# Optimization experiments

Measured on AMD Instinct MI355X. Metric: run time of the kernel, lower is better.

Reference implementation:

```python
import jax, jax.numpy as jnp
import numpy as np

N_NODES = 10000
HEADS = 4
NEG_SLOPE = 0.2


def gat_conv(x, src, dst, W, att_src, att_dst, bias, heads, ch):
    # x: [N, F_in]; W: [F_in, heads*ch]; att_*: [heads, ch]; bias: [heads*ch]
    N = x.shape[0]
    h = (x @ W).reshape(N, heads, ch)                       # [N, H, C]
    a_s = jnp.einsum('nhc,hc->nh', h, att_src)              # [N, H]
    a_d = jnp.einsum('nhc,hc->nh', h, att_dst)              # [N, H]
    e = jax.nn.leaky_relu(a_s[src] + a_d[dst], NEG_SLOPE)   # [E, H]
    # segment softmax over incoming edges of each dst node
    m = jax.ops.segment_max(e, dst, num_segments=N)         # [N, H]
    e = jnp.exp(e - m[dst])
    denom = jax.ops.segment_sum(e, dst, num_segments=N)     # [N, H]
    alpha = e / (denom[dst] + 1e-16)                        # [E, H]
    msg = h[src] * alpha[:, :, None]                        # [E, H, C]
    out = jax.ops.segment_sum(msg, dst, num_segments=N)     # [N, H, C]
    return out.reshape(N, heads * ch) + bias                # concat heads


def setup_inputs() -> dict:
    key = jax.random.key(0)
    ks = jax.random.split(key, 12)
    in_c, hid, out_c, H = 256, 64, 64, HEADS
    n_edges = 320000
    x = jax.random.normal(ks[0], (N_NODES, in_c), dtype=jnp.float32)
    edge_index = jax.random.randint(ks[1], (2, n_edges), 0, N_NODES, dtype=jnp.int64)

    def glorot(k, shape):
        fan = shape[0] + shape[-1]
        s = jnp.sqrt(6.0 / fan)
        return jax.random.uniform(k, shape, jnp.float32, -s, s)

    return {
        'x': x, 'edge_index': edge_index,
        'W1': glorot(ks[2], (in_c, H * hid)),
        'a1s': glorot(ks[3], (H, hid)), 'a1d': glorot(ks[4], (H, hid)),
        'b1': jnp.zeros((H * hid,), jnp.float32),
        'W2': glorot(ks[5], (H * hid, H * hid)),
        'a2s': glorot(ks[6], (H, hid)), 'a2d': glorot(ks[7], (H, hid)),
        'b2': jnp.zeros((H * hid,), jnp.float32),
        'W3': glorot(ks[8], (H * hid, H * out_c)),
        'a3s': glorot(ks[9], (H, out_c)), 'a3d': glorot(ks[10], (H, out_c)),
        'b3': jnp.zeros((H * out_c,), jnp.float32),
    }


def reference(x, edge_index, W1, a1s, a1d, b1, W2, a2s, a2d, b2, W3, a3s, a3d, b3):
    N = x.shape[0]
    # PyG GATConv default: add self loops
    loops = jnp.arange(N, dtype=edge_index.dtype)
    src = jnp.concatenate([edge_index[0], loops])
    dst = jnp.concatenate([edge_index[1], loops])
    hid, out_c = 64, 64
    h1 = jax.nn.elu(gat_conv(x, src, dst, W1, a1s, a1d, b1, HEADS, hid))
    h2 = jax.nn.elu(gat_conv(h1, src, dst, W2, a2s, a2d, b2, HEADS, hid))
    oup = jax.nn.elu(gat_conv(h2, src, dst, W3, a3s, a3d, b3, HEADS, out_c))
    return oup
```

## Files before the change

kernel.cpp:

```cpp
#include <hip/hip_runtime.h>
#include <hip/hip_bf16.h>

typedef __hip_bfloat16 bf16;
typedef __bf16 bf16x8v __attribute__((ext_vector_type(8)));
typedef float f32x4 __attribute__((ext_vector_type(4)));
typedef unsigned short u16x8 __attribute__((ext_vector_type(8)));

#define CAP 128

__device__ __forceinline__ float bits2f(unsigned short u) {
  union { unsigned int i; float f; } c;
  c.i = ((unsigned int)u) << 16;
  return c.f;
}


__global__ void wt_zero_kernel(const float* __restrict__ W0, const float* __restrict__ W1,
                               const float* __restrict__ W2, bf16* __restrict__ Wt,
                               int* __restrict__ cnt, int N) {
  __shared__ float tile[16][17];
  int b = blockIdx.x;
  if (b < 768) {
    int L = b >> 8, rem = b & 255;
    const float* W = (L == 0) ? W0 : (L == 1) ? W1 : W2;
    bf16* T = Wt + (size_t)L * 65536;
    int n0 = (rem & 15) * 16, k0 = (rem >> 4) * 16;
    int tx = threadIdx.x & 15, ty = threadIdx.x >> 4;
    tile[ty][tx] = W[(k0 + ty) * 256 + n0 + tx];
    __syncthreads();
    T[(n0 + ty) * 256 + k0 + tx] = __float2bfloat16(tile[tx][ty]);
  } else {
    int idx = (b - 768) * 256 + threadIdx.x;
    if (idx < N) cnt[idx] = 0;
  }
}


template <bool FP32IN>
__device__ __forceinline__ void gemm_body(const void* __restrict__ Xv,
                                          const bf16* __restrict__ Wt,
                                          const float* __restrict__ att_s,
                                          const float* __restrict__ att_d,
                                          bf16* __restrict__ H, float* __restrict__ a_s,
                                          float* __restrict__ a_d, int M, int m0, int hd,
                                          bf16* As, bf16* Bs) {
  const int LDK = 136;
  int tid = threadIdx.x;
  int wave = tid >> 6, lane = tid & 63;
  int quad = lane >> 4, l16 = lane & 15;
  int n0 = hd * 64;
  int srow = tid >> 2;
  int koff = (tid & 3) * 32;

  const float* Xf = (const float*)Xv;
  const bf16*  Xb = (const bf16*)Xv;

  f32x4 acc[4] = {{0.f, 0.f, 0.f, 0.f}, {0.f, 0.f, 0.f, 0.f},
                  {0.f, 0.f, 0.f, 0.f}, {0.f, 0.f, 0.f, 0.f}};

  for (int ks = 0; ks < 256; ks += 128) {
    int gm = m0 + srow;
#pragma unroll
    for (int c = 0; c < 4; c++) {
      int ko = koff + c * 8;
      uint4 v;
      if (FP32IN) {
        float4 u0 = make_float4(0.f, 0.f, 0.f, 0.f), u1 = u0;
        if (gm < M) {
          u0 = *(const float4*)&Xf[gm * 256 + ks + ko];
          u1 = *(const float4*)&Xf[gm * 256 + ks + ko + 4];
        }
        union { bf16 h[8]; uint4 u; } pk;
        pk.h[0] = __float2bfloat16(u0.x); pk.h[1] = __float2bfloat16(u0.y);
        pk.h[2] = __float2bfloat16(u0.z); pk.h[3] = __float2bfloat16(u0.w);
        pk.h[4] = __float2bfloat16(u1.x); pk.h[5] = __float2bfloat16(u1.y);
        pk.h[6] = __float2bfloat16(u1.z); pk.h[7] = __float2bfloat16(u1.w);
        v = pk.u;
      } else {
        v = (gm < M) ? *(const uint4*)&Xb[gm * 256 + ks + ko]
                     : make_uint4(0u, 0u, 0u, 0u);
      }
      *(uint4*)&As[srow * LDK + ko] = v;
    }
#pragma unroll
    for (int c = 0; c < 4; c++) {
      int ko = koff + c * 8;
      *(uint4*)&Bs[srow * LDK + ko] = *(const uint4*)&Wt[(n0 + srow) * 256 + ks + ko];
    }
    __syncthreads();

#pragma unroll
    for (int kk = 0; kk < 4; kk++) {
      bf16x8v af = *(const bf16x8v*)&As[(wave * 16 + l16) * LDK + kk * 32 + quad * 8];
#pragma unroll
      for (int t = 0; t < 4; t++) {
        bf16x8v bfr = *(const bf16x8v*)&Bs[(t * 16 + l16) * LDK + kk * 32 + quad * 8];
        acc[t] = __builtin_amdgcn_mfma_f32_16x16x32_bf16(af, bfr, acc[t], 0, 0, 0);
      }
    }
    __syncthreads();
  }

  float ps[4] = {0.f, 0.f, 0.f, 0.f}, pd[4] = {0.f, 0.f, 0.f, 0.f};
#pragma unroll
  for (int t = 0; t < 4; t++) {
    float sa = att_s[hd * 64 + t * 16 + l16];
    float da = att_d[hd * 64 + t * 16 + l16];
#pragma unroll
    for (int j = 0; j < 4; j++) {
      int gm = m0 + wave * 16 + quad * 4 + j;
      float v = acc[t][j];
      if (gm < M) H[gm * 256 + n0 + t * 16 + l16] = __float2bfloat16(v);
      ps[j] += v * sa;
      pd[j] += v * da;
    }
  }
#pragma unroll
  for (int j = 0; j < 4; j++) {
#pragma unroll
    for (int s = 1; s < 16; s <<= 1) {
      ps[j] += __shfl_xor(ps[j], s, 64);
      pd[j] += __shfl_xor(pd[j], s, 64);
    }
    int gm = m0 + wave * 16 + quad * 4 + j;
    if (l16 == 0 && gm < M) {
      a_s[gm * 4 + hd] = ps[j];
      a_d[gm * 4 + hd] = pd[j];
    }
  }
}

__global__ void __launch_bounds__(256, 4)
gemm_mfma_kernel(const bf16* __restrict__ X, const bf16* __restrict__ Wt,
                 const float* __restrict__ att_s, const float* __restrict__ att_d,
                 bf16* __restrict__ H, float* __restrict__ a_s, float* __restrict__ a_d,
                 int M) {
  __shared__ bf16 As[64 * 136];
  __shared__ bf16 Bs[64 * 136];
  gemm_body<false>(X, Wt, att_s, att_d, H, a_s, a_d, M, blockIdx.x * 64, blockIdx.y,
                   As, Bs);
}

__global__ void __launch_bounds__(256, 4)
gemm1_fill_kernel(const float* __restrict__ X, const bf16* __restrict__ Wt,
                  const float* __restrict__ att_s, const float* __restrict__ att_d,
                  bf16* __restrict__ H, float* __restrict__ a_s, float* __restrict__ a_d,
                  int M, const int* __restrict__ ei, int E, int N,
                  int* __restrict__ cnt, int* __restrict__ csr, int ngb) {
  __shared__ bf16 As[64 * 136];
  __shared__ bf16 Bs[64 * 136];
  int b = blockIdx.x;
  if (b < ngb) {
    gemm_body<true>(X, Wt, att_s, att_d, H, a_s, a_d, M, (b >> 2) * 64, b & 3, As, Bs);
  } else {
    int t = (b - ngb) * 256 + threadIdx.x;
    if (t >= E + N) return;
    int src, dst;
    if (t < E) { src = ei[t]; dst = ei[E + t]; }
    else       { src = t - E; dst = t - E; }
    int pos = atomicAdd(&cnt[dst], 1);
    if (pos < CAP) csr[dst * CAP + pos] = src;
  }
}


template <bool FINAL>
__global__ void __launch_bounds__(256, 8)
agg_wave_kernel(const bf16* __restrict__ H, const float* __restrict__ a_s,
                const float* __restrict__ a_d, const int* __restrict__ cnt,
                const int* __restrict__ csr, const float* __restrict__ bias,
                bf16* __restrict__ OutB, float* __restrict__ OutF, int N) {
  __shared__ int   wIdx[4][128];
  __shared__ float wP[4][128 * 4];
  int tid = threadIdx.x;
  int wave = tid >> 6, lane = tid & 63;
  int n = blockIdx.x * 4 + wave;

  int deg = 0, degp = 0;
  if (n < N) {
    deg = min(cnt[n], CAP);
    degp = (deg + 7) & ~7;
    float4 ad4 = *(const float4*)&a_d[n * 4];
#pragma unroll
    for (int base = 0; base < 2; base++) {
      int jj = base * 64 + lane;
      if (jj < deg) {
        int src = csr[n * CAP + jj];
        wIdx[wave][jj] = src;
        float4 as4 = *(const float4*)&a_s[src * 4];
        float4 e;
        e.x = as4.x + ad4.x; e.x = (e.x > 0.f) ? e.x : 0.2f * e.x;
        e.y = as4.y + ad4.y; e.y = (e.y > 0.f) ? e.y : 0.2f * e.y;
        e.z = as4.z + ad4.z; e.z = (e.z > 0.f) ? e.z : 0.2f * e.z;
        e.w = as4.w + ad4.w; e.w = (e.w > 0.f) ? e.w : 0.2f * e.w;
        float4 pv;
        pv.x = __expf(e.x); pv.y = __expf(e.y);
        pv.z = __expf(e.z); pv.w = __expf(e.w);
        *(float4*)&wP[wave][jj * 4] = pv;
      }
    }
    int pad = degp - deg;
    if (lane < pad) {
      int jd = deg + lane;
      wIdx[wave][jd] = 0;
      *(float4*)&wP[wave][jd * 4] = make_float4(0.f, 0.f, 0.f, 0.f);
    }
  }
  __syncthreads();
  if (n >= N) return;

  int sel = lane >> 5;
  int l32 = lane & 31;
  int c8 = l32 * 8;
  int head = l32 >> 3;
  const unsigned short* Hs = (const unsigned short*)H;

  float acc[8] = {0.f, 0.f, 0.f, 0.f, 0.f, 0.f, 0.f, 0.f};
  float s = 0.f;
  int npairp = degp >> 1;

  for (int it = 0; it < npairp; it += 4) {
    int   jv[4]; int sv[4]; float pv[4]; u16x8 hv[4];
#pragma unroll
    for (int u = 0; u < 4; u++) jv[u] = 2 * (it + u) + sel;
#pragma unroll
    for (int u = 0; u < 4; u++) sv[u] = wIdx[wave][jv[u]];
#pragma unroll
    for (int u = 0; u < 4; u++) pv[u] = wP[wave][jv[u] * 4 + head];
#pragma unroll
    for (int u = 0; u < 4; u++) hv[u] = *(const u16x8*)(Hs + sv[u] * 256 + c8);
#pragma unroll
    for (int u = 0; u < 4; u++) {
      s += pv[u];
#pragma unroll
      for (int k = 0; k < 8; k++) acc[k] += pv[u] * bits2f(hv[u][k]);
    }
  }

  s += __shfl_xor(s, 32, 64);
#pragma unroll
  for (int k = 0; k < 8; k++) acc[k] += __shfl_xor(acc[k], 32, 64);

  if (sel == 0) {
    float inv = 1.f / (s + 1e-16f);
    float4 b0 = *(const float4*)&bias[c8];
    float4 b1 = *(const float4*)&bias[c8 + 4];
    float v[8];
    v[0] = acc[0] * inv + b0.x; v[1] = acc[1] * inv + b0.y;
    v[2] = acc[2] * inv + b0.z; v[3] = acc[3] * inv + b0.w;
    v[4] = acc[4] * inv + b1.x; v[5] = acc[5] * inv + b1.y;
    v[6] = acc[6] * inv + b1.z; v[7] = acc[7] * inv + b1.w;
#pragma unroll
    for (int k = 0; k < 8; k++) v[k] = (v[k] > 0.f) ? v[k] : expm1f(v[k]);
    if (FINAL) {
      *(float4*)&OutF[n * 256 + c8]     = make_float4(v[0], v[1], v[2], v[3]);
      *(float4*)&OutF[n * 256 + c8 + 4] = make_float4(v[4], v[5], v[6], v[7]);
    } else {
      union { bf16 h[8]; u16x8 u; } pk;
#pragma unroll
      for (int k = 0; k < 8; k++) pk.h[k] = __float2bfloat16(v[k]);
      *(u16x8*)((unsigned short*)OutB + n * 256 + c8) = pk.u;
    }
  }
}


extern "C" void kernel_launch(void* const* d_in, const int* in_sizes, int n_in,
                              void* d_out, int out_size, void* d_ws, size_t ws_size,
                              hipStream_t stream) {
  const int N = in_sizes[0] / 256;
  const int E = in_sizes[1] / 2;

  const float* x  = (const float*)d_in[0];
  const int*   ei = (const int*)d_in[1];
  const float* Wl[3]  = {(const float*)d_in[2], (const float*)d_in[6], (const float*)d_in[10]};
  const float* asl[3] = {(const float*)d_in[3], (const float*)d_in[7], (const float*)d_in[11]};
  const float* adl[3] = {(const float*)d_in[4], (const float*)d_in[8], (const float*)d_in[12]};
  const float* bl[3]  = {(const float*)d_in[5], (const float*)d_in[9], (const float*)d_in[13]};
  float* out = (float*)d_out;

  char* p = (char*)d_ws;
  auto carve = [&](size_t bytes) {
    char* r = p;
    p += (bytes + 255) & ~size_t(255);
    return r;
  };
  int*   cnt     = (int*)carve(sizeof(int) * N);
  int*   csr     = (int*)carve(sizeof(int) * N * CAP);
  float* a_s     = (float*)carve(sizeof(float) * N * 4);
  float* a_d     = (float*)carve(sizeof(float) * N * 4);
  bf16*  Wt      = (bf16*)carve(sizeof(bf16) * 3 * 65536);
  bf16*  h_buf   = (bf16*)carve(sizeof(bf16) * N * 256);
  bf16*  x_buf   = (bf16*)carve(sizeof(bf16) * N * 256);
  (void)ws_size; (void)n_in; (void)out_size;

  const int zb = (N + 255) / 256;
  const int eb = (E + N + 255) / 256;
  const int ngb = ((N + 63) / 64) * 4;
  const int ab = (N + 3) / 4;
  dim3 ggrid((N + 63) / 64, 4);

  wt_zero_kernel<<<768 + zb, 256, 0, stream>>>(Wl[0], Wl[1], Wl[2], Wt, cnt, N);
  gemm1_fill_kernel<<<ngb + eb, 256, 0, stream>>>(x, Wt, asl[0], adl[0], h_buf,
                                                  a_s, a_d, N, ei, E, N, cnt, csr, ngb);
  agg_wave_kernel<false><<<ab, 256, 0, stream>>>(h_buf, a_s, a_d, cnt, csr, bl[0],
                                                 x_buf, nullptr, N);
  gemm_mfma_kernel<<<ggrid, 256, 0, stream>>>(x_buf, Wt + 65536, asl[1], adl[1],
                                              h_buf, a_s, a_d, N);
  agg_wave_kernel<false><<<ab, 256, 0, stream>>>(h_buf, a_s, a_d, cnt, csr, bl[1],
                                                 x_buf, nullptr, N);
  gemm_mfma_kernel<<<ggrid, 256, 0, stream>>>(x_buf, Wt + 131072, asl[2], adl[2],
                                              h_buf, a_s, a_d, N);
  agg_wave_kernel<true><<<ab, 256, 0, stream>>>(h_buf, a_s, a_d, cnt, csr, bl[2],
                                                nullptr, out, N);
}
```

Baseline: 189.0 us.

## Fuse all GAT stages into one persistent cooperative kernel with grid syncs

```diff
diff --git a/kernel.cpp b/kernel.cpp
--- a/kernel.cpp
+++ b/kernel.cpp
@@ -1,5 +1,8 @@
 #include <hip/hip_runtime.h>
+#include <hip/hip_cooperative_groups.h>
 #include <hip/hip_bf16.h>
+
+namespace cg = cooperative_groups;
 
 typedef __hip_bfloat16 bf16;
 typedef __bf16 bf16x8v __attribute__((ext_vector_type(8)));
@@ -12,27 +15,6 @@
   union { unsigned int i; float f; } c;
   c.i = ((unsigned int)u) << 16;
   return c.f;
-}
-
-
-__global__ void wt_zero_kernel(const float* __restrict__ W0, const float* __restrict__ W1,
-                               const float* __restrict__ W2, bf16* __restrict__ Wt,
-                               int* __restrict__ cnt, int N) {
-  __shared__ float tile[16][17];
-  int b = blockIdx.x;
-  if (b < 768) {
-    int L = b >> 8, rem = b & 255;
-    const float* W = (L == 0) ? W0 : (L == 1) ? W1 : W2;
-    bf16* T = Wt + (size_t)L * 65536;
-    int n0 = (rem & 15) * 16, k0 = (rem >> 4) * 16;
-    int tx = threadIdx.x & 15, ty = threadIdx.x >> 4;
-    tile[ty][tx] = W[(k0 + ty) * 256 + n0 + tx];
-    __syncthreads();
-    T[(n0 + ty) * 256 + k0 + tx] = __float2bfloat16(tile[tx][ty]);
-  } else {
-    int idx = (b - 768) * 256 + threadIdx.x;
-    if (idx < N) cnt[idx] = 0;
-  }
 }
 
 
@@ -127,6 +109,210 @@
       a_s[gm * 4 + hd] = ps[j];
       a_d[gm * 4 + hd] = pd[j];
     }
+  }
+}
+
+
+__device__ __forceinline__ void agg_stage(const bf16* __restrict__ H,
+                                          const float* __restrict__ a_s,
+                                          const float* __restrict__ a_d,
+                                          const int* __restrict__ cnt,
+                                          const int* __restrict__ csr,
+                                          const float* __restrict__ bias,
+                                          bf16* __restrict__ OutB,
+                                          float* __restrict__ OutF, int N,
+                                          bool final_, char* smem, int blk, int nblk) {
+  int tid = threadIdx.x;
+  int wave = tid >> 6, lane = tid & 63;
+  int* wIdx = (int*)smem + wave * 128;
+  float* wP = (float*)(smem + 2048) + wave * 512;
+  int ngr = (N + 3) >> 2;
+  for (int ng = blk; ng < ngr; ng += nblk) {
+    int n = ng * 4 + wave;
+    int deg = 0, degp = 0;
+    if (n < N) {
+      deg = min(cnt[n], CAP);
+      degp = (deg + 7) & ~7;
+      float4 ad4 = *(const float4*)&a_d[n * 4];
+#pragma unroll
+      for (int base = 0; base < 2; base++) {
+        int jj = base * 64 + lane;
+        if (jj < deg) {
+          int src = csr[n * CAP + jj];
+          wIdx[jj] = src;
+          float4 as4 = *(const float4*)&a_s[src * 4];
+          float4 e;
+          e.x = as4.x + ad4.x; e.x = (e.x > 0.f) ? e.x : 0.2f * e.x;
+          e.y = as4.y + ad4.y; e.y = (e.y > 0.f) ? e.y : 0.2f * e.y;
+          e.z = as4.z + ad4.z; e.z = (e.z > 0.f) ? e.z : 0.2f * e.z;
+          e.w = as4.w + ad4.w; e.w = (e.w > 0.f) ? e.w : 0.2f * e.w;
+          float4 pv;
+          pv.x = __expf(e.x); pv.y = __expf(e.y);
+          pv.z = __expf(e.z); pv.w = __expf(e.w);
+          *(float4*)&wP[jj * 4] = pv;
+        }
+      }
+      int pad = degp - deg;
+      if (lane < pad) {
+        wIdx[deg + lane] = 0;
+        *(float4*)&wP[(deg + lane) * 4] = make_float4(0.f, 0.f, 0.f, 0.f);
+      }
+    }
+    __syncthreads();
+    if (n < N) {
+      int sel = lane >> 5;
+      int l32 = lane & 31;
+      int c8 = l32 * 8;
+      int head = l32 >> 3;
+      const unsigned short* Hs = (const unsigned short*)H;
+
+      float acc[8] = {0.f, 0.f, 0.f, 0.f, 0.f, 0.f, 0.f, 0.f};
+      float s = 0.f;
+      int npairp = degp >> 1;
+
+      for (int it = 0; it < npairp; it += 4) {
+        int jv[4]; int sv[4]; float pv[4]; u16x8 hv[4];
+#pragma unroll
+        for (int u = 0; u < 4; u++) jv[u] = 2 * (it + u) + sel;
+#pragma unroll
+        for (int u = 0; u < 4; u++) sv[u] = wIdx[jv[u]];
+#pragma unroll
+        for (int u = 0; u < 4; u++) pv[u] = wP[jv[u] * 4 + head];
+#pragma unroll
+        for (int u = 0; u < 4; u++) hv[u] = *(const u16x8*)(Hs + sv[u] * 256 + c8);
+#pragma unroll
+        for (int u = 0; u < 4; u++) {
+          s += pv[u];
+#pragma unroll
+          for (int k = 0; k < 8; k++) acc[k] += pv[u] * bits2f(hv[u][k]);
+        }
+      }
+
+      s += __shfl_xor(s, 32, 64);
+#pragma unroll
+      for (int k = 0; k < 8; k++) acc[k] += __shfl_xor(acc[k], 32, 64);
+
+      if (sel == 0) {
+        float inv = 1.f / (s + 1e-16f);
+        float4 b0 = *(const float4*)&bias[c8];
+        float4 b1 = *(const float4*)&bias[c8 + 4];
+        float v[8];
+        v[0] = acc[0] * inv + b0.x; v[1] = acc[1] * inv + b0.y;
+        v[2] = acc[2] * inv + b0.z; v[3] = acc[3] * inv + b0.w;
+        v[4] = acc[4] * inv + b1.x; v[5] = acc[5] * inv + b1.y;
+        v[6] = acc[6] * inv + b1.z; v[7] = acc[7] * inv + b1.w;
+#pragma unroll
+        for (int k = 0; k < 8; k++) v[k] = (v[k] > 0.f) ? v[k] : expm1f(v[k]);
+        if (final_) {
+          *(float4*)&OutF[n * 256 + c8]     = make_float4(v[0], v[1], v[2], v[3]);
+          *(float4*)&OutF[n * 256 + c8 + 4] = make_float4(v[4], v[5], v[6], v[7]);
+        } else {
+          union { bf16 h[8]; u16x8 u; } pk;
+#pragma unroll
+          for (int k = 0; k < 8; k++) pk.h[k] = __float2bfloat16(v[k]);
+          *(u16x8*)((unsigned short*)OutB + n * 256 + c8) = pk.u;
+        }
+      }
+    }
+  }
+}
+
+
+__global__ void __launch_bounds__(256, 4)
+uber_kernel(const float* __restrict__ x, const int* __restrict__ ei,
+            const float* __restrict__ W0, const float* __restrict__ as0,
+            const float* __restrict__ ad0, const float* __restrict__ bias0,
+            const float* __restrict__ W1, const float* __restrict__ as1,
+            const float* __restrict__ ad1, const float* __restrict__ bias1,
+            const float* __restrict__ W2, const float* __restrict__ as2,
+            const float* __restrict__ ad2, const float* __restrict__ bias2,
+            int* __restrict__ cnt, int* __restrict__ csr,
+            float* __restrict__ a_s, float* __restrict__ a_d,
+            bf16* __restrict__ Wt, bf16* __restrict__ h_buf,
+            bf16* __restrict__ x_buf, float* __restrict__ outp, int N, int E) {
+  cg::grid_group grid = cg::this_grid();
+  __shared__ char smem[34816];
+  bf16* As = (bf16*)smem;
+  bf16* Bs = (bf16*)smem + 64 * 136;
+  int nblk = (int)gridDim.x;
+  int blk = (int)blockIdx.x;
+  int tid = threadIdx.x;
+
+  {
+    float(*tile)[17] = (float(*)[17])smem;
+    int zb = (N + 255) >> 8;
+    for (int b = blk; b < 768 + zb; b += nblk) {
+      if (b < 768) {
+        int L = b >> 8, rem = b & 255;
+        const float* W = (L == 0) ? W0 : (L == 1) ? W1 : W2;
+        bf16* T = Wt + (size_t)L * 65536;
+        int n0 = (rem & 15) * 16, k0 = (rem >> 4) * 16;
+        int tx = tid & 15, ty = tid >> 4;
+        tile[ty][tx] = W[(k0 + ty) * 256 + n0 + tx];
+        __syncthreads();
+        T[(n0 + ty) * 256 + k0 + tx] = __float2bfloat16(tile[tx][ty]);
+      } else {
+        int idx = (b - 768) * 256 + tid;
+        if (idx < N) cnt[idx] = 0;
+      }
+      __syncthreads();
+    }
+  }
+  grid.sync();
+
+  int ngb = ((N + 63) >> 6) * 4;
+  for (int j = blk; j < ngb; j += nblk)
+    gemm_body<true>(x, Wt, as0, ad0, h_buf, a_s, a_d, N, (j >> 2) * 64, j & 3, As, Bs);
+  int eb = (E + N + 255) >> 8;
+  for (int j = blk; j < eb; j += nblk) {
+    int t = j * 256 + tid;
+    if (t < E + N) {
+      int s_, d_;
+      if (t < E) { s_ = ei[t]; d_ = ei[E + t]; }
+      else       { s_ = t - E; d_ = t - E; }
+      int pos = atomicAdd(&cnt[d_], 1);
+      if (pos < CAP) csr[d_ * CAP + pos] = s_;
+    }
+  }
+  grid.sync();
+
+  agg_stage(h_buf, a_s, a_d, cnt, csr, bias0, x_buf, nullptr, N, false, smem, blk, nblk);
+  grid.sync();
+
+  for (int j = blk; j < ngb; j += nblk)
+    gemm_body<false>(x_buf, Wt + 65536, as1, ad1, h_buf, a_s, a_d, N, (j >> 2) * 64,
+                     j & 3, As, Bs);
+  grid.sync();
+
+  agg_stage(h_buf, a_s, a_d, cnt, csr, bias1, x_buf, nullptr, N, false, smem, blk, nblk);
+  grid.sync();
+
+  for (int j = blk; j < ngb; j += nblk)
+    gemm_body<false>(x_buf, Wt + 131072, as2, ad2, h_buf, a_s, a_d, N, (j >> 2) * 64,
+                     j & 3, As, Bs);
+  grid.sync();
+
+  agg_stage(h_buf, a_s, a_d, cnt, csr, bias2, nullptr, outp, N, true, smem, blk, nblk);
+}
+
+
+__global__ void wt_zero_kernel(const float* __restrict__ W0, const float* __restrict__ W1,
+                               const float* __restrict__ W2, bf16* __restrict__ Wt,
+                               int* __restrict__ cnt, int N) {
+  __shared__ float tile[16][17];
+  int b = blockIdx.x;
+  if (b < 768) {
+    int L = b >> 8, rem = b & 255;
+    const float* W = (L == 0) ? W0 : (L == 1) ? W1 : W2;
+    bf16* T = Wt + (size_t)L * 65536;
+    int n0 = (rem & 15) * 16, k0 = (rem >> 4) * 16;
+    int tx = threadIdx.x & 15, ty = threadIdx.x >> 4;
+    tile[ty][tx] = W[(k0 + ty) * 256 + n0 + tx];
+    __syncthreads();
+    T[(n0 + ty) * 256 + k0 + tx] = __float2bfloat16(tile[tx][ty]);
+  } else {
+    int idx = (b - 768) * 256 + threadIdx.x;
+    if (idx < N) cnt[idx] = 0;
   }
 }
 
@@ -163,105 +349,15 @@
   }
 }
 
-
 template <bool FINAL>
 __global__ void __launch_bounds__(256, 8)
 agg_wave_kernel(const bf16* __restrict__ H, const float* __restrict__ a_s,
                 const float* __restrict__ a_d, const int* __restrict__ cnt,
                 const int* __restrict__ csr, const float* __restrict__ bias,
                 bf16* __restrict__ OutB, float* __restrict__ OutF, int N) {
-  __shared__ int   wIdx[4][128];
-  __shared__ float wP[4][128 * 4];
-  int tid = threadIdx.x;
-  int wave = tid >> 6, lane = tid & 63;
-  int n = blockIdx.x * 4 + wave;
-
-  int deg = 0, degp = 0;
-  if (n < N) {
-    deg = min(cnt[n], CAP);
-    degp = (deg + 7) & ~7;
-    float4 ad4 = *(const float4*)&a_d[n * 4];
-#pragma unroll
-    for (int base = 0; base < 2; base++) {
-      int jj = base * 64 + lane;
-      if (jj < deg) {
-        int src = csr[n * CAP + jj];
-        wIdx[wave][jj] = src;
-        float4 as4 = *(const float4*)&a_s[src * 4];
-        float4 e;
-        e.x = as4.x + ad4.x; e.x = (e.x > 0.f) ? e.x : 0.2f * e.x;
-        e.y = as4.y + ad4.y; e.y = (e.y > 0.f) ? e.y : 0.2f * e.y;
-        e.z = as4.z + ad4.z; e.z = (e.z > 0.f) ? e.z : 0.2f * e.z;
-        e.w = as4.w + ad4.w; e.w = (e.w > 0.f) ? e.w : 0.2f * e.w;
-        float4 pv;
-        pv.x = __expf(e.x); pv.y = __expf(e.y);
-        pv.z = __expf(e.z); pv.w = __expf(e.w);
-        *(float4*)&wP[wave][jj * 4] = pv;
-      }
-    }
-    int pad = degp - deg;
-    if (lane < pad) {
-      int jd = deg + lane;
-      wIdx[wave][jd] = 0;
-      *(float4*)&wP[wave][jd * 4] = make_float4(0.f, 0.f, 0.f, 0.f);
-    }
-  }
-  __syncthreads();
-  if (n >= N) return;
-
-  int sel = lane >> 5;
-  int l32 = lane & 31;
-  int c8 = l32 * 8;
-  int head = l32 >> 3;
-  const unsigned short* Hs = (const unsigned short*)H;
-
-  float acc[8] = {0.f, 0.f, 0.f, 0.f, 0.f, 0.f, 0.f, 0.f};
-  float s = 0.f;
-  int npairp = degp >> 1;
-
-  for (int it = 0; it < npairp; it += 4) {
-    int   jv[4]; int sv[4]; float pv[4]; u16x8 hv[4];
-#pragma unroll
-    for (int u = 0; u < 4; u++) jv[u] = 2 * (it + u) + sel;
-#pragma unroll
-    for (int u = 0; u < 4; u++) sv[u] = wIdx[wave][jv[u]];
-#pragma unroll
-    for (int u = 0; u < 4; u++) pv[u] = wP[wave][jv[u] * 4 + head];
-#pragma unroll
-    for (int u = 0; u < 4; u++) hv[u] = *(const u16x8*)(Hs + sv[u] * 256 + c8);
-#pragma unroll
-    for (int u = 0; u < 4; u++) {
-      s += pv[u];
-#pragma unroll
-      for (int k = 0; k < 8; k++) acc[k] += pv[u] * bits2f(hv[u][k]);
-    }
-  }
-
-  s += __shfl_xor(s, 32, 64);
-#pragma unroll
-  for (int k = 0; k < 8; k++) acc[k] += __shfl_xor(acc[k], 32, 64);
-
-  if (sel == 0) {
-    float inv = 1.f / (s + 1e-16f);
-    float4 b0 = *(const float4*)&bias[c8];
-    float4 b1 = *(const float4*)&bias[c8 + 4];
-    float v[8];
-    v[0] = acc[0] * inv + b0.x; v[1] = acc[1] * inv + b0.y;
-    v[2] = acc[2] * inv + b0.z; v[3] = acc[3] * inv + b0.w;
-    v[4] = acc[4] * inv + b1.x; v[5] = acc[5] * inv + b1.y;
-    v[6] = acc[6] * inv + b1.z; v[7] = acc[7] * inv + b1.w;
-#pragma unroll
-    for (int k = 0; k < 8; k++) v[k] = (v[k] > 0.f) ? v[k] : expm1f(v[k]);
-    if (FINAL) {
-      *(float4*)&OutF[n * 256 + c8]     = make_float4(v[0], v[1], v[2], v[3]);
-      *(float4*)&OutF[n * 256 + c8 + 4] = make_float4(v[4], v[5], v[6], v[7]);
-    } else {
-      union { bf16 h[8]; u16x8 u; } pk;
-#pragma unroll
-      for (int k = 0; k < 8; k++) pk.h[k] = __float2bfloat16(v[k]);
-      *(u16x8*)((unsigned short*)OutB + n * 256 + c8) = pk.u;
-    }
-  }
+  __shared__ char smem[10240];
+  agg_stage(H, a_s, a_d, cnt, csr, bias, OutB, OutF, N, FINAL, smem, blockIdx.x,
+            gridDim.x);
 }
 
 
@@ -273,10 +369,18 @@
 
   const float* x  = (const float*)d_in[0];
   const int*   ei = (const int*)d_in[1];
-  const float* Wl[3]  = {(const float*)d_in[2], (const float*)d_in[6], (const float*)d_in[10]};
-  const float* asl[3] = {(const float*)d_in[3], (const float*)d_in[7], (const float*)d_in[11]};
-  const float* adl[3] = {(const float*)d_in[4], (const float*)d_in[8], (const float*)d_in[12]};
-  const float* bl[3]  = {(const float*)d_in[5], (const float*)d_in[9], (const float*)d_in[13]};
+  const float* W0 = (const float*)d_in[2];
+  const float* as0 = (const float*)d_in[3];
+  const float* ad0 = (const float*)d_in[4];
+  const float* bz0 = (const float*)d_in[5];
+  const float* W1 = (const float*)d_in[6];
+  const float* as1 = (const float*)d_in[7];
+  const float* ad1 = (const float*)d_in[8];
+  const float* bz1 = (const float*)d_in[9];
+  const float* W2 = (const float*)d_in[10];
+  const float* as2 = (const float*)d_in[11];
+  const float* ad2 = (const float*)d_in[12];
+  const float* bz2 = (const float*)d_in[13];
   float* out = (float*)d_out;
 
   char* p = (char*)d_ws;
@@ -285,14 +389,36 @@
     p += (bytes + 255) & ~size_t(255);
     return r;
   };
-  int*   cnt     = (int*)carve(sizeof(int) * N);
-  int*   csr     = (int*)carve(sizeof(int) * N * CAP);
-  float* a_s     = (float*)carve(sizeof(float) * N * 4);
-  float* a_d     = (float*)carve(sizeof(float) * N * 4);
-  bf16*  Wt      = (bf16*)carve(sizeof(bf16) * 3 * 65536);
-  bf16*  h_buf   = (bf16*)carve(sizeof(bf16) * N * 256);
-  bf16*  x_buf   = (bf16*)carve(sizeof(bf16) * N * 256);
+  int*   cnt   = (int*)carve(sizeof(int) * N);
+  int*   csr   = (int*)carve(sizeof(int) * N * CAP);
+  float* a_s   = (float*)carve(sizeof(float) * N * 4);
+  float* a_d   = (float*)carve(sizeof(float) * N * 4);
+  bf16*  Wt    = (bf16*)carve(sizeof(bf16) * 3 * 65536);
+  bf16*  h_buf = (bf16*)carve(sizeof(bf16) * N * 256);
+  bf16*  x_buf = (bf16*)carve(sizeof(bf16) * N * 256);
   (void)ws_size; (void)n_in; (void)out_size;
+
+  int nb = 0;
+  if (hipOccupancyMaxActiveBlocksPerMultiprocessor(&nb, uber_kernel, 256, 0) !=
+          hipSuccess || nb < 1)
+    nb = 4;
+  if (nb > 4) nb = 4;
+  int devCU = 0, dev = 0;
+  hipGetDevice(&dev);
+  if (hipDeviceGetAttribute(&devCU, hipDeviceAttributeMultiprocessorCount, dev) !=
+          hipSuccess || devCU <= 0)
+    devCU = 256;
+  int gridX = devCU * nb;
+
+  int Ni = N, Ei = E;
+  void* args[] = {(void*)&x,   (void*)&ei,  (void*)&W0,  (void*)&as0, (void*)&ad0,
+                  (void*)&bz0, (void*)&W1,  (void*)&as1, (void*)&ad1, (void*)&bz1,
+                  (void*)&W2,  (void*)&as2, (void*)&ad2, (void*)&bz2, (void*)&cnt,
+                  (void*)&csr, (void*)&a_s, (void*)&a_d, (void*)&Wt,  (void*)&h_buf,
+                  (void*)&x_buf, (void*)&out, (void*)&Ni, (void*)&Ei};
+  hipError_t cerr = hipLaunchCooperativeKernel((const void*)uber_kernel, dim3(gridX),
+                                               dim3(256), args, 0, stream);
+  if (cerr == hipSuccess) return;
 
   const int zb = (N + 255) / 256;
   const int eb = (E + N + 255) / 256;
@@ -300,17 +426,17 @@
   const int ab = (N + 3) / 4;
   dim3 ggrid((N + 63) / 64, 4);
 
-  wt_zero_kernel<<<768 + zb, 256, 0, stream>>>(Wl[0], Wl[1], Wl[2], Wt, cnt, N);
-  gemm1_fill_kernel<<<ngb + eb, 256, 0, stream>>>(x, Wt, asl[0], adl[0], h_buf,
-                                                  a_s, a_d, N, ei, E, N, cnt, csr, ngb);
-  agg_wave_kernel<false><<<ab, 256, 0, stream>>>(h_buf, a_s, a_d, cnt, csr, bl[0],
-                                                 x_buf, nullptr, N);
-  gemm_mfma_kernel<<<ggrid, 256, 0, stream>>>(x_buf, Wt + 65536, asl[1], adl[1],
-                                              h_buf, a_s, a_d, N);
-  agg_wave_kernel<false><<<ab, 256, 0, stream>>>(h_buf, a_s, a_d, cnt, csr, bl[1],
-                                                 x_buf, nullptr, N);
-  gemm_mfma_kernel<<<ggrid, 256, 0, stream>>>(x_buf, Wt + 131072, asl[2], adl[2],
-                                              h_buf, a_s, a_d, N);
-  agg_wave_kernel<true><<<ab, 256, 0, stream>>>(h_buf, a_s, a_d, cnt, csr, bl[2],
-                                                nullptr, out, N);
-}
+  wt_zero_kernel<<<768 + zb, 256, 0, stream>>>(W0, W1, W2, Wt, cnt, N);
+  gemm1_fill_kernel<<<ngb + eb, 256, 0, stream>>>(x, Wt, as0, ad0, h_buf, a_s, a_d, N,
+                                                  ei, E, N, cnt, csr, ngb);
+  agg_wave_kernel<false><<<ab, 256, 0, stream>>>(h_buf, a_s, a_d, cnt, csr, bz0, x_buf,
+                                                 nullptr, N);
+  gemm_mfma_kernel<<<ggrid, 256, 0, stream>>>(x_buf, Wt + 65536, as1, ad1, h_buf, a_s,
+                                              a_d, N);
+  agg_wave_kernel<false><<<ab, 256, 0, stream>>>(h_buf, a_s, a_d, cnt, csr, bz1, x_buf,
+                                                 nullptr, N);
+  gemm_mfma_kernel<<<ggrid, 256, 0, stream>>>(x_buf, Wt + 131072, as2, ad2, h_buf, a_s,
+                                              a_d, N);
+  agg_wave_kernel<true><<<ab, 256, 0, stream>>>(h_buf, a_s, a_d, cnt, csr, bz2, nullptr,
+                                                out, N);
+}
```

Measured after the change: 601.7 us. +218.3%, slower.

## Fuse aggregation of layer L with GEMM of layer L+1 in one kernel

Applied to the files above, without the earlier changes.

```diff
diff --git a/kernel.cpp b/kernel.cpp
--- a/kernel.cpp
+++ b/kernel.cpp
@@ -128,17 +128,6 @@
       a_d[gm * 4 + hd] = pd[j];
     }
   }
-}
-
-__global__ void __launch_bounds__(256, 4)
-gemm_mfma_kernel(const bf16* __restrict__ X, const bf16* __restrict__ Wt,
-                 const float* __restrict__ att_s, const float* __restrict__ att_d,
-                 bf16* __restrict__ H, float* __restrict__ a_s, float* __restrict__ a_d,
-                 int M) {
-  __shared__ bf16 As[64 * 136];
-  __shared__ bf16 Bs[64 * 136];
-  gemm_body<false>(X, Wt, att_s, att_d, H, a_s, a_d, M, blockIdx.x * 64, blockIdx.y,
-                   As, Bs);
 }
 
 __global__ void __launch_bounds__(256, 4)
@@ -164,17 +153,175 @@
 }
 
 
-template <bool FINAL>
+__global__ void __launch_bounds__(256, 2)
+fused_ag_kernel(const bf16* __restrict__ Hin, const float* __restrict__ as_in,
+                const float* __restrict__ ad_in, const int* __restrict__ cnt,
+                const int* __restrict__ csr, const float* __restrict__ bias,
+                const bf16* __restrict__ Wtn, const float* __restrict__ att_s,
+                const float* __restrict__ att_d, bf16* __restrict__ Hout,
+                float* __restrict__ as_out, float* __restrict__ ad_out, int N) {
+  const int LDKF = 264;
+  const int LDK = 136;
+  __shared__ bf16 As[64 * 264];
+  __shared__ bf16 Bs[64 * 136];
+  int tid = threadIdx.x;
+  int wave = tid >> 6, lane = tid & 63;
+  int m0 = blockIdx.x * 64;
+
+  int*   wIdx = (int*)((char*)Bs + (size_t)wave * 512);
+  float* wP   = (float*)((char*)Bs + 2048 + (size_t)wave * 2048);
+  int sel = lane >> 5, l32 = lane & 31;
+  int c8 = l32 * 8, head = l32 >> 3;
+  const unsigned short* Hs = (const unsigned short*)Hin;
+
+  for (int r = 0; r < 16; r++) {
+    int n = m0 + r * 4 + wave;
+    int deg = 0, degp = 0;
+    if (n < N) {
+      deg = min(cnt[n], CAP);
+      degp = (deg + 7) & ~7;
+      float4 ad4 = *(const float4*)&ad_in[n * 4];
+#pragma unroll
+      for (int base = 0; base < 2; base++) {
+        int jj = base * 64 + lane;
+        if (jj < deg) {
+          int src = csr[n * CAP + jj];
+          wIdx[jj] = src;
+          float4 as4 = *(const float4*)&as_in[src * 4];
+          float4 e;
+          e.x = as4.x + ad4.x; e.x = (e.x > 0.f) ? e.x : 0.2f * e.x;
+          e.y = as4.y + ad4.y; e.y = (e.y > 0.f) ? e.y : 0.2f * e.y;
+          e.z = as4.z + ad4.z; e.z = (e.z > 0.f) ? e.z : 0.2f * e.z;
+          e.w = as4.w + ad4.w; e.w = (e.w > 0.f) ? e.w : 0.2f * e.w;
+          float4 pv;
+          pv.x = __expf(e.x); pv.y = __expf(e.y);
+          pv.z = __expf(e.z); pv.w = __expf(e.w);
+          *(float4*)&wP[jj * 4] = pv;
+        }
+      }
+      int pad = degp - deg;
+      if (lane < pad) {
+        wIdx[deg + lane] = 0;
+        *(float4*)&wP[(deg + lane) * 4] = make_float4(0.f, 0.f, 0.f, 0.f);
+      }
+    }
+    __syncthreads();
+    if (n < N) {
+      float acc[8] = {0.f, 0.f, 0.f, 0.f, 0.f, 0.f, 0.f, 0.f};
+      float s = 0.f;
+      int npairp = degp >> 1;
+      for (int it = 0; it < npairp; it += 4) {
+        int jv[4]; int sv[4]; float pv[4]; u16x8 hv[4];
+#pragma unroll
+        for (int u = 0; u < 4; u++) jv[u] = 2 * (it + u) + sel;
+#pragma unroll
+        for (int u = 0; u < 4; u++) sv[u] = wIdx[jv[u]];
+#pragma unroll
+        for (int u = 0; u < 4; u++) pv[u] = wP[jv[u] * 4 + head];
+#pragma unroll
+        for (int u = 0; u < 4; u++) hv[u] = *(const u16x8*)(Hs + sv[u] * 256 + c8);
+#pragma unroll
+        for (int u = 0; u < 4; u++) {
+          s += pv[u];
+#pragma unroll
+          for (int k = 0; k < 8; k++) acc[k] += pv[u] * bits2f(hv[u][k]);
+        }
+      }
+      s += __shfl_xor(s, 32, 64);
+#pragma unroll
+      for (int k = 0; k < 8; k++) acc[k] += __shfl_xor(acc[k], 32, 64);
+      if (sel == 0) {
+        float inv = 1.f / (s + 1e-16f);
+        float4 b0 = *(const float4*)&bias[c8];
+        float4 b1 = *(const float4*)&bias[c8 + 4];
+        float v[8];
+        v[0] = acc[0] * inv + b0.x; v[1] = acc[1] * inv + b0.y;
+        v[2] = acc[2] * inv + b0.z; v[3] = acc[3] * inv + b0.w;
+        v[4] = acc[4] * inv + b1.x; v[5] = acc[5] * inv + b1.y;
+        v[6] = acc[6] * inv + b1.z; v[7] = acc[7] * inv + b1.w;
+#pragma unroll
+        for (int k = 0; k < 8; k++) v[k] = (v[k] > 0.f) ? v[k] : expm1f(v[k]);
+        union { bf16 h[8]; u16x8 u; } pk;
+#pragma unroll
+        for (int k = 0; k < 8; k++) pk.h[k] = __float2bfloat16(v[k]);
+        *(u16x8*)&As[(r * 4 + wave) * LDKF + c8] = pk.u;
+      }
+    } else if (sel == 0) {
+      u16x8 z = {0, 0, 0, 0, 0, 0, 0, 0};
+      *(u16x8*)&As[(r * 4 + wave) * LDKF + c8] = z;
+    }
+    __syncthreads();
+  }
+
+  int quad = lane >> 4, l16 = lane & 15;
+  int srow = tid >> 2;
+  int koff = (tid & 3) * 32;
+
+  for (int hd = 0; hd < 4; hd++) {
+    int n0 = hd * 64;
+    f32x4 acc[4] = {{0.f, 0.f, 0.f, 0.f}, {0.f, 0.f, 0.f, 0.f},
+                    {0.f, 0.f, 0.f, 0.f}, {0.f, 0.f, 0.f, 0.f}};
+    for (int ks = 0; ks < 256; ks += 128) {
+#pragma unroll
+      for (int c = 0; c < 4; c++) {
+        int ko = koff + c * 8;
+        *(uint4*)&Bs[srow * LDK + ko] = *(const uint4*)&Wtn[(n0 + srow) * 256 + ks + ko];
+      }
+      __syncthreads();
+#pragma unroll
+      for (int kk = 0; kk < 4; kk++) {
+        bf16x8v af = *(const bf16x8v*)&As[(wave * 16 + l16) * LDKF + ks + kk * 32 + quad * 8];
+#pragma unroll
+        for (int t = 0; t < 4; t++) {
+          bf16x8v bfr = *(const bf16x8v*)&Bs[(t * 16 + l16) * LDK + kk * 32 + quad * 8];
+          acc[t] = __builtin_amdgcn_mfma_f32_16x16x32_bf16(af, bfr, acc[t], 0, 0, 0);
+        }
+      }
+      __syncthreads();
+    }
+    float ps[4] = {0.f, 0.f, 0.f, 0.f}, pd[4] = {0.f, 0.f, 0.f, 0.f};
+#pragma unroll
+    for (int t = 0; t < 4; t++) {
+      float sa = att_s[hd * 64 + t * 16 + l16];
+      float da = att_d[hd * 64 + t * 16 + l16];
+#pragma unroll
+      for (int j = 0; j < 4; j++) {
+        int gm = m0 + wave * 16 + quad * 4 + j;
+        float v = acc[t][j];
+        if (gm < N) Hout[gm * 256 + n0 + t * 16 + l16] = __float2bfloat16(v);
+        ps[j] += v * sa;
+        pd[j] += v * da;
+      }
+    }
+#pragma unroll
+    for (int j = 0; j < 4; j++) {
+#pragma unroll
+      for (int s = 1; s < 16; s <<= 1) {
+        ps[j] += __shfl_xor(ps[j], s, 64);
+        pd[j] += __shfl_xor(pd[j], s, 64);
+      }
+      int gm = m0 + wave * 16 + quad * 4 + j;
+      if (l16 == 0 && gm < N) {
+        as_out[gm * 4 + hd] = ps[j];
+        ad_out[gm * 4 + hd] = pd[j];
+      }
+    }
+  }
+}
+
+
 __global__ void __launch_bounds__(256, 8)
-agg_wave_kernel(const bf16* __restrict__ H, const float* __restrict__ a_s,
-                const float* __restrict__ a_d, const int* __restrict__ cnt,
-                const int* __restrict__ csr, const float* __restrict__ bias,
-                bf16* __restrict__ OutB, float* __restrict__ OutF, int N) {
-  __shared__ int   wIdx[4][128];
-  __shared__ float wP[4][128 * 4];
+agg_final_kernel(const bf16* __restrict__ H, const float* __restrict__ a_s,
+                 const float* __restrict__ a_d, const int* __restrict__ cnt,
+                 const int* __restrict__ csr, const float* __restrict__ bias,
+                 float* __restrict__ OutF, int N) {
+  __shared__ int   wIdxS[4][128];
+  __shared__ float wPS[4][512];
   int tid = threadIdx.x;
   int wave = tid >> 6, lane = tid & 63;
   int n = blockIdx.x * 4 + wave;
+  int* wIdx = wIdxS[wave];
+  float* wP = wPS[wave];
 
   int deg = 0, degp = 0;
   if (n < N) {
@@ -186,7 +333,7 @@
       int jj = base * 64 + lane;
       if (jj < deg) {
         int src = csr[n * CAP + jj];
-        wIdx[wave][jj] = src;
+        wIdx[jj] = src;
         float4 as4 = *(const float4*)&a_s[src * 4];
         float4 e;
         e.x = as4.x + ad4.x; e.x = (e.x > 0.f) ? e.x : 0.2f * e.x;
@@ -196,14 +343,13 @@
         float4 pv;
         pv.x = __expf(e.x); pv.y = __expf(e.y);
         pv.z = __expf(e.z); pv.w = __expf(e.w);
-        *(float4*)&wP[wave][jj * 4] = pv;
+        *(float4*)&wP[jj * 4] = pv;
       }
     }
     int pad = degp - deg;
     if (lane < pad) {
-      int jd = deg + lane;
-      wIdx[wave][jd] = 0;
-      *(float4*)&wP[wave][jd * 4] = make_float4(0.f, 0.f, 0.f, 0.f);
+      wIdx[deg + lane] = 0;
+      *(float4*)&wP[(deg + lane) * 4] = make_float4(0.f, 0.f, 0.f, 0.f);
     }
   }
   __syncthreads();
@@ -220,13 +366,13 @@
   int npairp = degp >> 1;
 
   for (int it = 0; it < npairp; it += 4) {
-    int   jv[4]; int sv[4]; float pv[4]; u16x8 hv[4];
+    int jv[4]; int sv[4]; float pv[4]; u16x8 hv[4];
 #pragma unroll
     for (int u = 0; u < 4; u++) jv[u] = 2 * (it + u) + sel;
 #pragma unroll
-    for (int u = 0; u < 4; u++) sv[u] = wIdx[wave][jv[u]];
-#pragma unroll
-    for (int u = 0; u < 4; u++) pv[u] = wP[wave][jv[u] * 4 + head];
+    for (int u = 0; u < 4; u++) sv[u] = wIdx[jv[u]];
+#pragma unroll
+    for (int u = 0; u < 4; u++) pv[u] = wP[jv[u] * 4 + head];
 #pragma unroll
     for (int u = 0; u < 4; u++) hv[u] = *(const u16x8*)(Hs + sv[u] * 256 + c8);
 #pragma unroll
@@ -252,15 +398,8 @@
     v[6] = acc[6] * inv + b1.z; v[7] = acc[7] * inv + b1.w;
 #pragma unroll
     for (int k = 0; k < 8; k++) v[k] = (v[k] > 0.f) ? v[k] : expm1f(v[k]);
-    if (FINAL) {
-      *(float4*)&OutF[n * 256 + c8]     = make_float4(v[0], v[1], v[2], v[3]);
-      *(float4*)&OutF[n * 256 + c8 + 4] = make_float4(v[4], v[5], v[6], v[7]);
-    } else {
-      union { bf16 h[8]; u16x8 u; } pk;
-#pragma unroll
-      for (int k = 0; k < 8; k++) pk.h[k] = __float2bfloat16(v[k]);
-      *(u16x8*)((unsigned short*)OutB + n * 256 + c8) = pk.u;
-    }
+    *(float4*)&OutF[n * 256 + c8]     = make_float4(v[0], v[1], v[2], v[3]);
+    *(float4*)&OutF[n * 256 + c8 + 4] = make_float4(v[4], v[5], v[6], v[7]);
   }
 }
 
@@ -285,32 +424,31 @@
     p += (bytes + 255) & ~size_t(255);
     return r;
   };
-  int*   cnt     = (int*)carve(sizeof(int) * N);
-  int*   csr     = (int*)carve(sizeof(int) * N * CAP);
-  float* a_s     = (float*)carve(sizeof(float) * N * 4);
-  float* a_d     = (float*)carve(sizeof(float) * N * 4);
-  bf16*  Wt      = (bf16*)carve(sizeof(bf16) * 3 * 65536);
-  bf16*  h_buf   = (bf16*)carve(sizeof(bf16) * N * 256);
-  bf16*  x_buf   = (bf16*)carve(sizeof(bf16) * N * 256);
+  int*   cnt   = (int*)carve(sizeof(int) * N);
+  int*   csr   = (int*)carve(sizeof(int) * N * CAP);
+  float* a_s   = (float*)carve(sizeof(float) * N * 4);
+  float* a_d   = (float*)carve(sizeof(float) * N * 4);
+  float* a_s2  = (float*)carve(sizeof(float) * N * 4);
+  float* a_d2  = (float*)carve(sizeof(float) * N * 4);
+  bf16*  Wt    = (bf16*)carve(sizeof(bf16) * 3 * 65536);
+  bf16*  h_buf = (bf16*)carve(sizeof(bf16) * N * 256);
+  bf16*  h2buf = (bf16*)carve(sizeof(bf16) * N * 256);
   (void)ws_size; (void)n_in; (void)out_size;
 
   const int zb = (N + 255) / 256;
   const int eb = (E + N + 255) / 256;
   const int ngb = ((N + 63) / 64) * 4;
+  const int fb = (N + 63) / 64;
   const int ab = (N + 3) / 4;
-  dim3 ggrid((N + 63) / 64, 4);
 
   wt_zero_kernel<<<768 + zb, 256, 0, stream>>>(Wl[0], Wl[1], Wl[2], Wt, cnt, N);
   gemm1_fill_kernel<<<ngb + eb, 256, 0, stream>>>(x, Wt, asl[0], adl[0], h_buf,
                                                   a_s, a_d, N, ei, E, N, cnt, csr, ngb);
-  agg_wave_kernel<false><<<ab, 256, 0, stream>>>(h_buf, a_s, a_d, cnt, csr, bl[0],
-                                                 x_buf, nullptr, N);
-  gemm_mfma_kernel<<<ggrid, 256, 0, stream>>>(x_buf, Wt + 65536, asl[1], adl[1],
-                                              h_buf, a_s, a_d, N);
-  agg_wave_kernel<false><<<ab, 256, 0, stream>>>(h_buf, a_s, a_d, cnt, csr, bl[1],
-                                                 x_buf, nullptr, N);
-  gemm_mfma_kernel<<<ggrid, 256, 0, stream>>>(x_buf, Wt + 131072, asl[2], adl[2],
-                                              h_buf, a_s, a_d, N);
-  agg_wave_kernel<true><<<ab, 256, 0, stream>>>(h_buf, a_s, a_d, cnt, csr, bl[2],
-                                                nullptr, out, N);
-}
+  fused_ag_kernel<<<fb, 256, 0, stream>>>(h_buf, a_s, a_d, cnt, csr, bl[0],
+                                          Wt + 65536, asl[1], adl[1],
+                                          h2buf, a_s2, a_d2, N);
+  fused_ag_kernel<<<fb, 256, 0, stream>>>(h2buf, a_s2, a_d2, cnt, csr, bl[1],
+                                          Wt + 131072, asl[2], adl[2],
+                                          h_buf, a_s, a_d, N);
+  agg_final_kernel<<<ab, 256, 0, stream>>>(h_buf, a_s, a_d, cnt, csr, bl[2], out, N);
+}
```

Result: slower. 288.7 us (+52.7%).

## Fold weight transpose into first GEMM launch and drop agg block barrier

Applied to the files above, without the earlier changes.

```diff
diff --git a/kernel.cpp b/kernel.cpp
--- a/kernel.cpp
+++ b/kernel.cpp
@@ -15,30 +15,9 @@
 }
 
 
-__global__ void wt_zero_kernel(const float* __restrict__ W0, const float* __restrict__ W1,
-                               const float* __restrict__ W2, bf16* __restrict__ Wt,
-                               int* __restrict__ cnt, int N) {
-  __shared__ float tile[16][17];
-  int b = blockIdx.x;
-  if (b < 768) {
-    int L = b >> 8, rem = b & 255;
-    const float* W = (L == 0) ? W0 : (L == 1) ? W1 : W2;
-    bf16* T = Wt + (size_t)L * 65536;
-    int n0 = (rem & 15) * 16, k0 = (rem >> 4) * 16;
-    int tx = threadIdx.x & 15, ty = threadIdx.x >> 4;
-    tile[ty][tx] = W[(k0 + ty) * 256 + n0 + tx];
-    __syncthreads();
-    T[(n0 + ty) * 256 + k0 + tx] = __float2bfloat16(tile[tx][ty]);
-  } else {
-    int idx = (b - 768) * 256 + threadIdx.x;
-    if (idx < N) cnt[idx] = 0;
-  }
-}
-
-
-template <bool FP32IN>
+template <bool FP32IN, bool WF32>
 __device__ __forceinline__ void gemm_body(const void* __restrict__ Xv,
-                                          const bf16* __restrict__ Wt,
+                                          const void* __restrict__ Wv,
                                           const float* __restrict__ att_s,
                                           const float* __restrict__ att_d,
                                           bf16* __restrict__ H, float* __restrict__ a_s,
@@ -54,6 +33,8 @@
 
   const float* Xf = (const float*)Xv;
   const bf16*  Xb = (const bf16*)Xv;
+  const float* Wf = (const float*)Wv;
+  const bf16*  Wb = (const bf16*)Wv;
 
   f32x4 acc[4] = {{0.f, 0.f, 0.f, 0.f}, {0.f, 0.f, 0.f, 0.f},
                   {0.f, 0.f, 0.f, 0.f}, {0.f, 0.f, 0.f, 0.f}};
@@ -82,10 +63,19 @@
       }
       *(uint4*)&As[srow * LDK + ko] = v;
     }
-#pragma unroll
-    for (int c = 0; c < 4; c++) {
-      int ko = koff + c * 8;
-      *(uint4*)&Bs[srow * LDK + ko] = *(const uint4*)&Wt[(n0 + srow) * 256 + ks + ko];
+    if (WF32) {
+      int tn = tid & 63, kq = tid >> 6;
+#pragma unroll
+      for (int i = 0; i < 32; i++) {
+        int kk2 = kq * 32 + i;
+        Bs[tn * LDK + kk2] = __float2bfloat16(Wf[(size_t)(ks + kk2) * 256 + n0 + tn]);
+      }
+    } else {
+#pragma unroll
+      for (int c = 0; c < 4; c++) {
+        int ko = koff + c * 8;
+        *(uint4*)&Bs[srow * LDK + ko] = *(const uint4*)&Wb[(n0 + srow) * 256 + ks + ko];
+      }
     }
     __syncthreads();
 
@@ -137,22 +127,26 @@
                  int M) {
   __shared__ bf16 As[64 * 136];
   __shared__ bf16 Bs[64 * 136];
-  gemm_body<false>(X, Wt, att_s, att_d, H, a_s, a_d, M, blockIdx.x * 64, blockIdx.y,
-                   As, Bs);
+  gemm_body<false, false>(X, Wt, att_s, att_d, H, a_s, a_d, M, blockIdx.x * 64,
+                          blockIdx.y, As, Bs);
 }
 
 __global__ void __launch_bounds__(256, 4)
-gemm1_fill_kernel(const float* __restrict__ X, const bf16* __restrict__ Wt,
+gemm1_fill_kernel(const float* __restrict__ X, const float* __restrict__ W0,
                   const float* __restrict__ att_s, const float* __restrict__ att_d,
                   bf16* __restrict__ H, float* __restrict__ a_s, float* __restrict__ a_d,
                   int M, const int* __restrict__ ei, int E, int N,
-                  int* __restrict__ cnt, int* __restrict__ csr, int ngb) {
+                  int* __restrict__ cnt, int* __restrict__ csr, int ngb, int eb,
+                  const float* __restrict__ W1, const float* __restrict__ W2,
+                  bf16* __restrict__ Wt) {
   __shared__ bf16 As[64 * 136];
   __shared__ bf16 Bs[64 * 136];
+  __shared__ float tile[16][17];
   int b = blockIdx.x;
   if (b < ngb) {
-    gemm_body<true>(X, Wt, att_s, att_d, H, a_s, a_d, M, (b >> 2) * 64, b & 3, As, Bs);
-  } else {
+    gemm_body<true, true>(X, W0, att_s, att_d, H, a_s, a_d, M, (b >> 2) * 64, b & 3,
+                          As, Bs);
+  } else if (b < ngb + eb) {
     int t = (b - ngb) * 256 + threadIdx.x;
     if (t >= E + N) return;
     int src, dst;
@@ -160,6 +154,16 @@
     else       { src = t - E; dst = t - E; }
     int pos = atomicAdd(&cnt[dst], 1);
     if (pos < CAP) csr[dst * CAP + pos] = src;
+  } else {
+    int b2 = b - ngb - eb;
+    int L = 1 + (b2 >> 8), rem = b2 & 255;
+    const float* W = (L == 1) ? W1 : W2;
+    bf16* T = Wt + (size_t)L * 65536;
+    int n0 = (rem & 15) * 16, k0 = (rem >> 4) * 16;
+    int tx = threadIdx.x & 15, ty = threadIdx.x >> 4;
+    tile[ty][tx] = W[(k0 + ty) * 256 + n0 + tx];
+    __syncthreads();
+    T[(n0 + ty) * 256 + k0 + tx] = __float2bfloat16(tile[tx][ty]);
   }
 }
 
@@ -170,23 +174,25 @@
                 const float* __restrict__ a_d, const int* __restrict__ cnt,
                 const int* __restrict__ csr, const float* __restrict__ bias,
                 bf16* __restrict__ OutB, float* __restrict__ OutF, int N) {
-  __shared__ int   wIdx[4][128];
-  __shared__ float wP[4][128 * 4];
+  __shared__ int   wIdxS[4][128];
+  __shared__ float wPS[4][512];
   int tid = threadIdx.x;
   int wave = tid >> 6, lane = tid & 63;
   int n = blockIdx.x * 4 + wave;
-
-  int deg = 0, degp = 0;
-  if (n < N) {
-    deg = min(cnt[n], CAP);
-    degp = (deg + 7) & ~7;
+  int* wIdx = wIdxS[wave];
+  float* wP = wPS[wave];
+  if (n >= N) return;
+
+  int deg = min(cnt[n], CAP);
+  int degp = (deg + 7) & ~7;
+  {
     float4 ad4 = *(const float4*)&a_d[n * 4];
 #pragma unroll
     for (int base = 0; base < 2; base++) {
       int jj = base * 64 + lane;
       if (jj < deg) {
         int src = csr[n * CAP + jj];
-        wIdx[wave][jj] = src;
+        wIdx[jj] = src;
         float4 as4 = *(const float4*)&a_s[src * 4];
         float4 e;
         e.x = as4.x + ad4.x; e.x = (e.x > 0.f) ? e.x : 0.2f * e.x;
@@ -196,18 +202,17 @@
         float4 pv;
         pv.x = __expf(e.x); pv.y = __expf(e.y);
         pv.z = __expf(e.z); pv.w = __expf(e.w);
-        *(float4*)&wP[wave][jj * 4] = pv;
+        *(float4*)&wP[jj * 4] = pv;
       }
     }
     int pad = degp - deg;
     if (lane < pad) {
-      int jd = deg + lane;
-      wIdx[wave][jd] = 0;
-      *(float4*)&wP[wave][jd * 4] = make_float4(0.f, 0.f, 0.f, 0.f);
-    }
-  }
-  __syncthreads();
-  if (n >= N) return;
+      wIdx[deg + lane] = 0;
+      *(float4*)&wP[(deg + lane) * 4] = make_float4(0.f, 0.f, 0.f, 0.f);
+    }
+  }
+  asm volatile("s_waitcnt lgkmcnt(0)" ::: "memory");
+  __builtin_amdgcn_sched_barrier(0);
 
   int sel = lane >> 5;
   int l32 = lane & 31;
@@ -220,13 +225,13 @@
   int npairp = degp >> 1;
 
   for (int it = 0; it < npairp; it += 4) {
-    int   jv[4]; int sv[4]; float pv[4]; u16x8 hv[4];
+    int jv[4]; int sv[4]; float pv[4]; u16x8 hv[4];
 #pragma unroll
     for (int u = 0; u < 4; u++) jv[u] = 2 * (it + u) + sel;
 #pragma unroll
-    for (int u = 0; u < 4; u++) sv[u] = wIdx[wave][jv[u]];
-#pragma unroll
-    for (int u = 0; u < 4; u++) pv[u] = wP[wave][jv[u] * 4 + head];
+    for (int u = 0; u < 4; u++) sv[u] = wIdx[jv[u]];
+#pragma unroll
+    for (int u = 0; u < 4; u++) pv[u] = wP[jv[u] * 4 + head];
 #pragma unroll
     for (int u = 0; u < 4; u++) hv[u] = *(const u16x8*)(Hs + sv[u] * 256 + c8);
 #pragma unroll
@@ -285,24 +290,24 @@
     p += (bytes + 255) & ~size_t(255);
     return r;
   };
-  int*   cnt     = (int*)carve(sizeof(int) * N);
-  int*   csr     = (int*)carve(sizeof(int) * N * CAP);
-  float* a_s     = (float*)carve(sizeof(float) * N * 4);
-  float* a_d     = (float*)carve(sizeof(float) * N * 4);
-  bf16*  Wt      = (bf16*)carve(sizeof(bf16) * 3 * 65536);
-  bf16*  h_buf   = (bf16*)carve(sizeof(bf16) * N * 256);
-  bf16*  x_buf   = (bf16*)carve(sizeof(bf16) * N * 256);
+  int*   cnt   = (int*)carve(sizeof(int) * N);
+  int*   csr   = (int*)carve(sizeof(int) * N * CAP);
+  float* a_s   = (float*)carve(sizeof(float) * N * 4);
+  float* a_d   = (float*)carve(sizeof(float) * N * 4);
+  bf16*  Wt    = (bf16*)carve(sizeof(bf16) * 3 * 65536);
+  bf16*  h_buf = (bf16*)carve(sizeof(bf16) * N * 256);
+  bf16*  x_buf = (bf16*)carve(sizeof(bf16) * N * 256);
   (void)ws_size; (void)n_in; (void)out_size;
 
-  const int zb = (N + 255) / 256;
-  const int eb = (E + N + 255) / 256;
+  const int eb  = (E + N + 255) / 256;
   const int ngb = ((N + 63) / 64) * 4;
-  const int ab = (N + 3) / 4;
+  const int ab  = (N + 3) / 4;
   dim3 ggrid((N + 63) / 64, 4);
 
-  wt_zero_kernel<<<768 + zb, 256, 0, stream>>>(Wl[0], Wl[1], Wl[2], Wt, cnt, N);
-  gemm1_fill_kernel<<<ngb + eb, 256, 0, stream>>>(x, Wt, asl[0], adl[0], h_buf,
-                                                  a_s, a_d, N, ei, E, N, cnt, csr, ngb);
+  hipMemsetAsync(cnt, 0, sizeof(int) * N, stream);
+  gemm1_fill_kernel<<<ngb + eb + 512, 256, 0, stream>>>(
+      x, Wl[0], asl[0], adl[0], h_buf, a_s, a_d, N, ei, E, N, cnt, csr, ngb, eb,
+      Wl[1], Wl[2], Wt);
   agg_wave_kernel<false><<<ab, 256, 0, stream>>>(h_buf, a_s, a_d, cnt, csr, bl[0],
                                                  x_buf, nullptr, N);
   gemm_mfma_kernel<<<ggrid, 256, 0, stream>>>(x_buf, Wt + 65536, asl[1], adl[1],
```

Measured after the change: 189.8 us (median of 3 runs). No clear change (+0.4%).
